# Kernel tuning notes

Hardware: AMD Instinct MI355X
Metric: run time of the kernel (lower is better)

## Reference

```python
import jax, jax.numpy as jnp
import numpy as np


def setup_inputs() -> dict:
    key = jax.random.key(0)
    k1, k2 = jax.random.split(key)
    B, L, D = 32, 1024, 512
    x = jax.random.normal(k1, (B, L, D), dtype=jnp.float32)
    durations = jax.random.randint(k2, (B, L), 0, 8, dtype=jnp.int64)
    return {"x": x, "durations": durations, "max_len": 4096}


def reference(x, durations, max_len):
    # Length regulation: repeat token i of row b durations[b,i] times along time,
    # pad/truncate to max_len. Implemented as cumsum + searchsorted gather
    # (single-pass, no host round-trip, no repeat_interleave).
    B, L, D = x.shape
    dur = jnp.maximum(durations, 0)
    cum = jnp.cumsum(dur, axis=1)            # [B, L] exclusive upper bounds per token
    t = jnp.arange(max_len)                  # [T] output frame indices
    # frame t belongs to token idx where cum[idx-1] <= t < cum[idx]
    idx = jax.vmap(lambda c: jnp.searchsorted(c, t, side='right'))(cum)  # [B, T]
    idx = jnp.clip(idx, 0, L - 1)
    out = jnp.take_along_axis(x, idx[:, :, None], axis=1)               # [B, T, D]
    valid = t[None, :] < cum[:, -1:]          # frames past total duration are zero-padded
    return out * valid[:, :, None].astype(x.dtype)
```

## Files before the change

### kernel.cpp

```cpp
#include <hip/hip_runtime.h>


#define B_ 32
#define L_ 1024
#define D_ 512
#define T_ 4096
#define TPC 8
#define NCHUNK (L_ / TPC)
#define NZ 16

typedef float fx4 __attribute__((ext_vector_type(4)));

__global__ __launch_bounds__(256) void lr_scan(const int* __restrict__ dur,
                                               int* __restrict__ cumg) {
    __shared__ int wsum[4];
    const int b = blockIdx.x;
    const int tid = threadIdx.x;

    int4 dv = reinterpret_cast<const int4*>(dur + b * L_)[tid];
    const int a0 = max(dv.x, 0), a1 = max(dv.y, 0);
    const int a2 = max(dv.z, 0), a3 = max(dv.w, 0);
    const int tsum = a0 + a1 + a2 + a3;

    int v = tsum;
    const int lane = tid & 63;
    #pragma unroll
    for (int off = 1; off < 64; off <<= 1) {
        int n = __shfl_up(v, off, 64);
        if (lane >= off) v += n;
    }
    const int wv = tid >> 6;
    if (lane == 63) wsum[wv] = v;
    __syncthreads();
    int woff = 0;
    #pragma unroll
    for (int w = 0; w < 3; ++w)
        if (w < wv) woff += wsum[w];
    const int incl = v + woff;
    const int e = incl - tsum;

    int4 cv;
    cv.x = e + a0; cv.y = e + a0 + a1; cv.z = e + a0 + a1 + a2; cv.w = incl;
    reinterpret_cast<int4*>(cumg + b * L_)[tid] = cv;
}

__global__ __launch_bounds__(256) void lr_scatter(const float* __restrict__ x,
                                                  const int* __restrict__ cumg,
                                                  float* __restrict__ out) {
    const int tid = threadIdx.x;
    const int slot = tid & 127;
    const int fhalf = tid >> 7;
    fx4* o = reinterpret_cast<fx4*>(out);

    if (blockIdx.x < B_ * NCHUNK) {
        const int b = blockIdx.x >> 7;
        const int c = blockIdx.x & (NCHUNK - 1);
        const int k0 = c * TPC;

        __shared__ int S[TPC + 1];
        if (tid <= TPC) {
            const int q = k0 + tid - 1;
            S[tid] = (q < 0) ? 0 : cumg[b * L_ + q];
        }
        __syncthreads();

        const fx4* xb = reinterpret_cast<const fx4*>(x) + (size_t)b * (L_ * D_ / 4);

        #pragma unroll
        for (int j = 0; j < TPC; ++j) {
            int lo = S[j], hi = S[j + 1];
            if (lo >= T_) break;
            if (hi > T_) hi = T_;
            if (lo >= hi) continue;
            const fx4 v = xb[(k0 + j) * 128 + slot];
            for (int f = lo + fhalf; f < hi; f += 2)
                __builtin_nontemporal_store(v, &o[((size_t)(b * T_ + f)) * 128 + slot]);
        }
    } else {
        const int z = blockIdx.x - B_ * NCHUNK;
        const int b = z >> 4;
        const int seg = z & (NZ - 1);
        const int total = cumg[b * L_ + L_ - 1];
        int lo = seg * (T_ / NZ);
        const int hi = lo + (T_ / NZ);
        if (lo < total) lo = total;
        const fx4 zv = {0.f, 0.f, 0.f, 0.f};
        for (int f = lo + fhalf; f < hi; f += 2)
            __builtin_nontemporal_store(zv, &o[((size_t)(b * T_ + f)) * 128 + slot]);
    }
}

extern "C" void kernel_launch(void* const* d_in, const int* in_sizes, int n_in,
                              void* d_out, int out_size, void* d_ws, size_t ws_size,
                              hipStream_t stream) {
    const float* x = (const float*)d_in[0];
    const int* dur = (const int*)d_in[1];
    float* out = (float*)d_out;
    int* cumg = (int*)d_ws;

    lr_scan<<<B_, 256, 0, stream>>>(dur, cumg);
    lr_scatter<<<B_ * NCHUNK + B_ * NZ, 256, 0, stream>>>(x, cumg, out);
}
```

Measured before the change: 70.89 us.

## Switch scatter to output-frame-parallel gather with per-block binary search

Replaces the token-chunk scatter, whose per-block work varied with the durations, plus its separate zero-padding blocks, with an output-driven gather. Each of 2048 blocks owns 64 output frames of one row. It loads the row's cumulative sums into shared memory, binary-searches the source token for each frame, then writes every frame exactly once, reloading x only when the token changes. This evens out the work per block and removes the divergent duration-dependent loops. In exchange, every block reads a full 4 KB cum row and runs a 10-step search.

```diff
diff --git a/kernel.cpp b/kernel.cpp
--- a/kernel.cpp
+++ b/kernel.cpp
@@ -5,9 +5,6 @@
 #define L_ 1024
 #define D_ 512
 #define T_ 4096
-#define TPC 8
-#define NCHUNK (L_ / TPC)
-#define NZ 16
 
 typedef float fx4 __attribute__((ext_vector_type(4)));
 
@@ -47,46 +44,53 @@
 __global__ __launch_bounds__(256) void lr_scatter(const float* __restrict__ x,
                                                   const int* __restrict__ cumg,
                                                   float* __restrict__ out) {
+    __shared__ int cum[L_];
+    __shared__ int ids[64];
     const int tid = threadIdx.x;
+    const int b = blockIdx.x >> 6;
+    const int f0 = (blockIdx.x & 63) * 64;
+
+    reinterpret_cast<int4*>(cum)[tid] =
+        reinterpret_cast<const int4*>(cumg + b * L_)[tid];
+    __syncthreads();
+
+    if (tid < 64) {
+        const int t = f0 + tid;
+        int idx = -1;
+        if (t < cum[L_ - 1]) {
+            idx = 0;
+            #pragma unroll
+            for (int s = 512; s > 0; s >>= 1)
+                if (cum[idx + s - 1] <= t) idx += s;
+        }
+        ids[tid] = idx;
+    }
+    __syncthreads();
+
     const int slot = tid & 127;
     const int fhalf = tid >> 7;
+
+    const fx4* xb = reinterpret_cast<const fx4*>(x) + (size_t)b * (L_ * D_ / 4);
     fx4* o = reinterpret_cast<fx4*>(out);
 
-    if (blockIdx.x < B_ * NCHUNK) {
-        const int b = blockIdx.x >> 7;
-        const int c = blockIdx.x & (NCHUNK - 1);
-        const int k0 = c * TPC;
+    #pragma unroll
+    for (int c = 0; c < 2; ++c) {
+        const int chunk = blockIdx.x * 2 + c;
+        fx4* ob = o + (size_t)chunk * 32 * 128;
 
-        __shared__ int S[TPC + 1];
-        if (tid <= TPC) {
-            const int q = k0 + tid - 1;
-            S[tid] = (q < 0) ? 0 : cumg[b * L_ + q];
+        int prev = -2;
+        fx4 v = {0.f, 0.f, 0.f, 0.f};
+        #pragma unroll
+        for (int i2 = 0; i2 < 16; ++i2) {
+            const int fi = 2 * i2 + fhalf;
+            const int id = ids[c * 32 + fi];
+            if (id != prev) {
+                if (id >= 0) v = xb[id * 128 + slot];
+                else         v = (fx4){0.f, 0.f, 0.f, 0.f};
+                prev = id;
+            }
+            __builtin_nontemporal_store(v, &ob[fi * 128 + slot]);
         }
-        __syncthreads();
-
-        const fx4* xb = reinterpret_cast<const fx4*>(x) + (size_t)b * (L_ * D_ / 4);
-
-        #pragma unroll
-        for (int j = 0; j < TPC; ++j) {
-            int lo = S[j], hi = S[j + 1];
-            if (lo >= T_) break;
-            if (hi > T_) hi = T_;
-            if (lo >= hi) continue;
-            const fx4 v = xb[(k0 + j) * 128 + slot];
-            for (int f = lo + fhalf; f < hi; f += 2)
-                __builtin_nontemporal_store(v, &o[((size_t)(b * T_ + f)) * 128 + slot]);
-        }
-    } else {
-        const int z = blockIdx.x - B_ * NCHUNK;
-        const int b = z >> 4;
-        const int seg = z & (NZ - 1);
-        const int total = cumg[b * L_ + L_ - 1];
-        int lo = seg * (T_ / NZ);
-        const int hi = lo + (T_ / NZ);
-        if (lo < total) lo = total;
-        const fx4 zv = {0.f, 0.f, 0.f, 0.f};
-        for (int f = lo + fhalf; f < hi; f += 2)
-            __builtin_nontemporal_store(zv, &o[((size_t)(b * T_ + f)) * 128 + slot]);
     }
 }
 
@@ -99,5 +103,5 @@
     int* cumg = (int*)d_ws;
 
     lr_scan<<<B_, 256, 0, stream>>>(dur, cumg);
-    lr_scatter<<<B_ * NCHUNK + B_ * NZ, 256, 0, stream>>>(x, cumg, out);
+    lr_scatter<<<2048, 256, 0, stream>>>(x, cumg, out);
 }
```

Measured after the change: 64.19 us. 1.1x faster.
